# Optimization experiments

Measured on AMD Instinct MI355X. Metric: run time of the kernel, lower is better.

## Reference

```python
import jax, jax.numpy as jnp
import numpy as np

T_SEQ = 120
BATCH = 256
HID = 512
D_LAG = 32
D_COV = 32
D_OUT = 1
N_LAYERS = 2
D_IN0 = D_LAG + D_COV
BN_EPS = 1e-5
SCALE_EPS = 1e-6
GAMMA = 1.0


def _gru_layer(x, Wih, Whh, bih, bhh):
    # x: [B, T, D] -> [B, T, H]; PyTorch GRU gate order (r, z, n)
    H = Whh.shape[1]
    gx = jnp.einsum('btd,gd->btg', x, Wih) + bih  # [B, T, 3H]
    gx_t = jnp.swapaxes(gx, 0, 1)                 # [T, B, 3H]
    h0 = jnp.zeros((x.shape[0], H), x.dtype)

    def step(h, g):
        gh = h @ Whh.T + bhh
        r = jax.nn.sigmoid(g[:, :H] + gh[:, :H])
        z = jax.nn.sigmoid(g[:, H:2 * H] + gh[:, H:2 * H])
        n = jnp.tanh(g[:, 2 * H:] + r * gh[:, 2 * H:])
        h = (1.0 - z) * n + z * h
        return h, h

    _, hs = jax.lax.scan(step, h0, gx_t)
    return jnp.swapaxes(hs, 0, 1)  # [B, T, H]


def setup_inputs() -> dict:
    key = jax.random.key(0)
    ks = jax.random.split(key, 16)
    s = 1.0 / np.sqrt(HID)
    inp = {
        'X_emb': jnp.zeros((T_SEQ, BATCH, 1), dtype=jnp.int32),
        'X_cov': jax.random.normal(ks[0], (T_SEQ, BATCH, D_COV), dtype=jnp.float32),
        'X_lag': jax.random.normal(ks[1], (T_SEQ, BATCH, D_LAG), dtype=jnp.float32),
        'y': jax.random.normal(ks[2], (T_SEQ, BATCH, D_OUT), dtype=jnp.float32),
        'd_outputseqlen': 24,
        'len_win': 30,
        'W_ih0': jax.random.uniform(ks[3], (3 * HID, D_IN0), minval=-s, maxval=s),
        'W_hh0': jax.random.uniform(ks[4], (3 * HID, HID), minval=-s, maxval=s),
        'b_ih0': jax.random.uniform(ks[5], (3 * HID,), minval=-s, maxval=s),
        'b_hh0': jax.random.uniform(ks[6], (3 * HID,), minval=-s, maxval=s),
        'W_ih1': jax.random.uniform(ks[7], (3 * HID, HID), minval=-s, maxval=s),
        'W_hh1': jax.random.uniform(ks[8], (3 * HID, HID), minval=-s, maxval=s),
        'b_ih1': jax.random.uniform(ks[9], (3 * HID,), minval=-s, maxval=s),
        'b_hh1': jax.random.uniform(ks[10], (3 * HID,), minval=-s, maxval=s),
        'gate_W': jax.random.normal(ks[11], (N_LAYERS, T_SEQ, T_SEQ * 2 * HID)) * 0.05,
        'gate_b': jnp.zeros((N_LAYERS, T_SEQ)),
        'bn_gamma': jnp.ones((N_LAYERS, T_SEQ)),
        'bn_beta': jnp.zeros((N_LAYERS, T_SEQ)),
        'fc_W': jax.random.uniform(ks[12], (D_OUT, HID), minval=-s, maxval=s),
        'fc_b': jnp.zeros((D_OUT,)),
    }
    return inp


def reference(X_emb, X_cov, X_lag, y, d_outputseqlen, len_win,
              W_ih0, W_hh0, b_ih0, b_hh0, W_ih1, W_hh1, b_ih1, b_hh1,
              gate_W, gate_b, bn_gamma, bn_beta, fc_W, fc_b):
    T, B, _ = X_lag.shape
    half = B // 2
    x = jnp.concatenate([X_lag, X_cov], axis=-1)   # [T, B, D]
    x = jnp.transpose(x, (1, 0, 2))                # [B, T, D]

    gru_params = [(W_ih0, W_hh0, b_ih0, b_hh0), (W_ih1, W_hh1, b_ih1, b_hh1)]
    outs = []
    gate_weights = []
    for l, (Wih, Whh, bih, bhh) in enumerate(gru_params):
        x = _gru_layer(x, Wih, Whh, bih, bhh)      # [B, T, H]
        outs.append(x)
        # process_gate_weight: src/tgt halves concatenated on feature dim
        x_all = jnp.concatenate([x[:half], x[half:]], axis=2).reshape(half, -1)  # [B/2, T*2H]
        z = x_all @ gate_W[l].T + gate_b[l]        # [B/2, T]
        m = z.mean(axis=0)
        v = ((z - m) ** 2).mean(axis=0)            # biased var (BatchNorm training mode)
        w = jax.nn.sigmoid(bn_gamma[l] * (z - m) / jnp.sqrt(v + BN_EPS) + bn_beta[l])
        gate_weights.append(jax.nn.softmax(w.mean(axis=0)))  # [T]

    # prediction head (original uses fc_scale for both loc and scale)
    fea = outs[-1]
    lin = fea[:, -d_outputseqlen:, :] @ fc_W.T + fc_b          # [B, L, D_OUT]
    y_hat_loc = jnp.transpose(lin, (1, 0, 2))                  # [L, B, D_OUT]
    y_hat_scale = jnp.transpose(jax.nn.softplus(lin), (1, 0, 2)) + SCALE_EPS
    y_t = y[-d_outputseqlen:]
    log_prob = (-0.5 * ((y_t - y_hat_loc) / y_hat_scale) ** 2
                - jnp.log(y_hat_scale) - 0.5 * jnp.log(2.0 * jnp.pi))
    loss_y = -log_prob.mean()

    # linear-MMD transfer loss over windowed (j, k) pairs, all layers
    idx = jnp.arange(T)
    mask = (jnp.abs(idx[:, None] - idx[None, :]) <= len_win).astype(fea.dtype)  # [T, T]
    loss_transfer = jnp.zeros(())
    for l, o in enumerate(outs):
        ms = o[:half].mean(axis=0)   # [T, H]
        mt = o[half:].mean(axis=0)   # [T, H]
        # D[j,k] = ||ms[j]-mt[k]||^2 == linear MMD of columns j (src) and k (tgt)
        D = ((ms ** 2).sum(-1)[:, None] + (mt ** 2).sum(-1)[None, :]
             - 2.0 * ms @ mt.T)
        loss_transfer = loss_transfer + jnp.dot(gate_weights[l], (mask * D).sum(axis=1))
    total_loss = loss_y + GAMMA * loss_transfer
    return (total_loss, loss_y, y_hat_loc, y_hat_scale, jnp.stack(gate_weights))
```

## Files before the change

### kernel.cpp

```cpp
#include <hip/hip_runtime.h>
#include <math.h>

#define T_SEQ 120
#define BATCH 256
#define HID   512
#define G3    1536
#define MROWS (BATCH*T_SEQ)
#define TS    (T_SEQ*HID)
#define KGATE 122880
#define FSTRIDE 16
#define NEGINF (-2147483647)

typedef __attribute__((ext_vector_type(8))) short bf16x8;
typedef __attribute__((ext_vector_type(4))) float f32x4;

__device__ __forceinline__ unsigned short f2bf(float f) {
    union { float f; unsigned u; } x; x.f = f;
    unsigned r = x.u + 0x7fffu + ((x.u >> 16) & 1u);
    return (unsigned short)(r >> 16);
}
__device__ __forceinline__ float bf2f(unsigned short u) {
    union { unsigned u; float f; } x; x.u = ((unsigned)u) << 16; return x.f;
}
__device__ __forceinline__ float sigm_fast(float x) {
    return 1.f / (1.f + __expf(-x));
}
__device__ __forceinline__ float tanh_fast(float x) {
    float e = __expf(2.f * x);
    return 1.f - 2.f / (e + 1.f);
}

__global__ void build_x(const float* __restrict__ X_lag,
                        const float* __restrict__ X_cov,
                        float* __restrict__ x_in)
{
    int idx = blockIdx.x * 256 + threadIdx.x;
    int d = idx & 63;
    int m = idx >> 6;
    int b = m / 120, t = m - b * 120;
    float v;
    if (d < 32) v = X_lag[((size_t)t * BATCH + b) * 32 + d];
    else        v = X_cov[((size_t)t * BATCH + b) * 32 + (d - 32)];
    x_in[idx] = v;
}

__global__ void cast_whh0(const float* __restrict__ W, unsigned short* __restrict__ o)
{
    int i = blockIdx.x * 256 + threadIdx.x;
    o[i] = f2bf(W[i]);
}

__global__ void cast_wcat1(const float* __restrict__ Whh, const float* __restrict__ Wih,
                           unsigned short* __restrict__ o)
{
    int i = blockIdx.x * 256 + threadIdx.x;
    int row = i >> 10, c = i & 1023;
    float v = (c < 512) ? Whh[row * 512 + c] : Wih[row * 512 + (c - 512)];
    o[i] = f2bf(v);
}

__global__ void mkbias(const float* __restrict__ bih0, const float* __restrict__ bhh0,
                       const float* __restrict__ bih1, const float* __restrict__ bhh1,
                       float* __restrict__ bcomb0, float* __restrict__ bc1)
{
    int n = blockIdx.x * 256 + threadIdx.x;
    bcomb0[n] = bih0[n] + (n < 1024 ? bhh0[n] : 0.f);
    bc1[n]    = bih1[n] + (n < 1024 ? bhh1[n] : 0.f);
}

__global__ __launch_bounds__(256) void gemm_abt_t(
    const float* __restrict__ A, const float* __restrict__ B,
    const float* __restrict__ bias, unsigned short* __restrict__ C,
    int M, int N, int K)
{
    __shared__ float As[32][129];
    __shared__ float Bs[32][129];
    int m0 = blockIdx.x * 128;
    int n0 = blockIdx.y * 128;
    int tid = threadIdx.x;
    int tx = tid & 15, ty = tid >> 4;
    float acc[8][8] = {};
    for (int k0 = 0; k0 < K; k0 += 32) {
        #pragma unroll
        for (int i = 0; i < 16; i++) {
            int e = tid + i * 256;
            int row = e >> 5, col = e & 31;
            As[col][row] = A[(size_t)(m0 + row) * K + k0 + col];
            Bs[col][row] = B[(size_t)(n0 + row) * K + k0 + col];
        }
        __syncthreads();
        #pragma unroll
        for (int kk = 0; kk < 32; kk++) {
            float a[8], b[8];
            #pragma unroll
            for (int i = 0; i < 8; i++) a[i] = As[kk][ty + i * 16];
            #pragma unroll
            for (int j = 0; j < 8; j++) b[j] = Bs[kk][tx + j * 16];
            #pragma unroll
            for (int i = 0; i < 8; i++)
                #pragma unroll
                for (int j = 0; j < 8; j++) acc[i][j] += a[i] * b[j];
        }
        __syncthreads();
    }
    #pragma unroll
    for (int i = 0; i < 8; i++) {
        int m = m0 + ty + i * 16;
        int b = m / 120, t = m - b * 120;
        #pragma unroll
        for (int j = 0; j < 8; j++) {
            int n = n0 + tx + j * 16;
            C[((size_t)t * 256 + b) * G3 + n] = f2bf(acc[i][j] + bias[n]);
        }
    }
}

__device__ __forceinline__ bool wait2(const int* __restrict__ f0b,
                                      const int* __restrict__ f1b,
                                      int thr0, int thr1, int lane)
{
    const int* ap; int thr;
    if (lane < 16)      { ap = f0b + lane * FSTRIDE;        thr = thr0; }
    else if (lane < 32) { ap = f1b + (lane - 16) * FSTRIDE; thr = thr1; }
    else                { ap = f0b;                         thr = NEGINF; }
    for (int it = 0; it < 50000; ++it) {
        int v = __hip_atomic_load(ap, __ATOMIC_RELAXED, __HIP_MEMORY_SCOPE_AGENT);
        if (__all(v >= thr)) return true;
        __builtin_amdgcn_s_sleep(1);
    }
    return false;
}

__global__ __launch_bounds__(256) void gru_xcd(
    const unsigned short* __restrict__ gx0,
    const unsigned short* __restrict__ Whh0,
    const unsigned short* __restrict__ Wcat1,
    const float* __restrict__ bhh0,
    const float* __restrict__ bc1,
    const float* __restrict__ bhh1,
    unsigned short* __restrict__ out0,
    unsigned short* __restrict__ out1,
    int* __restrict__ flags,
    int* __restrict__ rolecnt)
{
    __shared__ unsigned short wlds[96 * 520];
    __shared__ int role_s;

    int xcd;
    asm("s_getreg_b32 %0, hwreg(20, 0, 32)" : "=s"(xcd));
    xcd &= 7;
    if (threadIdx.x == 0) role_s = atomicAdd(&rolecnt[xcd * 16], 1);
    __syncthreads();
    const int role = role_s;
    if (role >= 32) return;

    const int layer = role >> 4;
    const int jb    = role & 15;
    const int j0    = jb * 32;
    const int tid   = threadIdx.x;
    const int w     = tid >> 6, lane = tid & 63;
    const int l15   = lane & 15, l4 = lane >> 4;
    const int jt    = w & 1, bt = w >> 1;
    const int jloc  = jt * 16 + l15;
    const int j     = j0 + jloc;
    const int bloc0 = bt * 16;
    const int bg0   = xcd * 32;

    {
        const unsigned short* Wsrc = layer ? Wcat1 : Whh0;
        const int wstr = layer ? 1024 : 512;
        for (int c = tid; c < 96 * 64; c += 256) {
            int lr = c >> 6, ck = c & 63;
            int grow = (lr >> 5) * 512 + j0 + (lr & 31);
            bf16x8 v = *(const bf16x8*)(Wsrc + (size_t)grow * wstr + ck * 8);
            *(bf16x8*)&wlds[lr * 520 + ck * 8] = v;
        }
    }
    float bn_, br_ = 0.f, bz_ = 0.f, bnx_ = 0.f;
    if (layer) { br_ = bc1[j]; bz_ = bc1[512 + j]; bnx_ = bc1[1024 + j]; bn_ = bhh1[1024 + j]; }
    else       { bn_ = bhh0[1024 + j]; }
    float carry[4] = {0.f, 0.f, 0.f, 0.f};

    const int* f0b = flags + (0 * 8 + xcd) * 16 * FSTRIDE;
    const int* f1b = flags + (1 * 8 + xcd) * 16 * FSTRIDE;
    int* myf = flags + ((layer * 8 + xcd) * 16 + jb) * FSTRIDE;
    __syncthreads();

    for (int t = 0; t < T_SEQ; t++) {
        bool ok = layer ? wait2(f0b, f1b, t, t - 1, lane)
                        : wait2(f0b, f1b, t - 1, NEGINF, lane);
        if (!ok) break;

        f32x4 a0 = {0,0,0,0}, a1 = {0,0,0,0}, a2 = {0,0,0,0}, a3 = {0,0,0,0};
        if (t > 0) {
            const unsigned short* hp = layer ? out1 : out0;
            #pragma unroll
            for (int ks = 0; ks < 16; ks++) {
                const int ko = ks * 32 + 8 * l4;
                bf16x8 A = *(const bf16x8*)(hp + ((size_t)(bg0 + bloc0 + l15) * T_SEQ + (t - 1)) * 512 + ko);
                bf16x8 B0 = *(const bf16x8*)&wlds[(0 * 32 + jloc) * 520 + ko];
                bf16x8 B1 = *(const bf16x8*)&wlds[(1 * 32 + jloc) * 520 + ko];
                bf16x8 B2 = *(const bf16x8*)&wlds[(2 * 32 + jloc) * 520 + ko];
                a0 = __builtin_amdgcn_mfma_f32_16x16x32_bf16(A, B0, a0, 0, 0, 0);
                a1 = __builtin_amdgcn_mfma_f32_16x16x32_bf16(A, B1, a1, 0, 0, 0);
                a2 = __builtin_amdgcn_mfma_f32_16x16x32_bf16(A, B2, a2, 0, 0, 0);
            }
        }
        if (layer) {
            #pragma unroll
            for (int ks = 0; ks < 16; ks++) {
                const int ko = ks * 32 + 8 * l4;
                bf16x8 A = *(const bf16x8*)(out0 + ((size_t)(bg0 + bloc0 + l15) * T_SEQ + t) * 512 + ko);
                const unsigned short* wb = Wcat1 + (size_t)j * 1024 + 512 + ko;
                bf16x8 B0 = *(const bf16x8*)(wb);
                bf16x8 B1 = *(const bf16x8*)(wb + 512 * 1024);
                bf16x8 B2 = *(const bf16x8*)(wb + 1024 * 1024);
                a0 = __builtin_amdgcn_mfma_f32_16x16x32_bf16(A, B0, a0, 0, 0, 0);
                a1 = __builtin_amdgcn_mfma_f32_16x16x32_bf16(A, B1, a1, 0, 0, 0);
                a3 = __builtin_amdgcn_mfma_f32_16x16x32_bf16(A, B2, a3, 0, 0, 0);
            }
        }
        unsigned short* op = layer ? out1 : out0;
        #pragma unroll
        for (int rr = 0; rr < 4; rr++) {
            int b = bg0 + bloc0 + 4 * l4 + rr;
            float pr, pz, pnx;
            if (!layer) {
                const unsigned short* gp = gx0 + ((size_t)t * 256 + b) * G3 + j;
                pr  = bf2f(gp[0])    + a0[rr];
                pz  = bf2f(gp[512])  + a1[rr];
                pnx = bf2f(gp[1024]);
            } else {
                pr = a0[rr] + br_; pz = a1[rr] + bz_; pnx = a3[rr] + bnx_;
            }
            float r = sigm_fast(pr);
            float z = sigm_fast(pz);
            float n = tanh_fast(pnx + r * (a2[rr] + bn_));
            float h = (1.f - z) * n + z * carry[rr];
            carry[rr] = h;
            op[((size_t)b * T_SEQ + t) * 512 + j] = f2bf(h);
        }
        asm volatile("s_waitcnt vmcnt(0)" ::: "memory");
        __syncthreads();
        if (tid == 0)
            __hip_atomic_store(myf, t, __ATOMIC_RELAXED, __HIP_MEMORY_SCOPE_AGENT);
    }
}

__global__ __launch_bounds__(256) void zpart_kernel(
    const unsigned short* __restrict__ out, const float* __restrict__ Gw,
    float* __restrict__ zp)
{
    __shared__ float Os[128][33];
    __shared__ float Gs[128][33];
    int bk = blockIdx.x;
    int t = bk >> 3, half = (bk >> 2) & 1, cq = bk & 3;
    int tid = threadIdx.x;
    int tx = tid & 15, ty = tid >> 4;
    float acc[8][8] = {};
    int cbase = cq * 128;
    for (int c0 = cbase; c0 < cbase + 128; c0 += 32) {
        #pragma unroll
        for (int i = 0; i < 16; i++) {
            int e = tid + i * 256;
            int row = e >> 5, col = e & 31;
            Os[row][col] = bf2f(out[((size_t)(row + half * 128) * T_SEQ + t) * 512 + c0 + col]);
            float v = 0.f;
            if (row < 120)
                v = Gw[(size_t)row * KGATE + (size_t)t * 1024 + half * 512 + c0 + col];
            Gs[row][col] = v;
        }
        __syncthreads();
        #pragma unroll
        for (int kk = 0; kk < 32; kk++) {
            float a[8], g[8];
            #pragma unroll
            for (int i = 0; i < 8; i++) a[i] = Os[ty + i * 16][kk];
            #pragma unroll
            for (int j = 0; j < 8; j++) g[j] = Gs[tx + j * 16][kk];
            #pragma unroll
            for (int i = 0; i < 8; i++)
                #pragma unroll
                for (int j = 0; j < 8; j++) acc[i][j] += a[i] * g[j];
        }
        __syncthreads();
    }
    float* zb = zp + (size_t)bk * (128 * 120);
    #pragma unroll
    for (int i = 0; i < 8; i++) {
        int ii = ty + i * 16;
        #pragma unroll
        for (int j = 0; j < 8; j++) {
            int r = tx + j * 16;
            if (r < 120) zb[ii * 120 + r] = acc[i][j];
        }
    }
}

__global__ void zreduce(const float* __restrict__ zp,
                        const float* __restrict__ gate_b_l,
                        float* __restrict__ z)
{
    int idx = blockIdx.x * 256 + threadIdx.x;
    if (idx >= 128 * 120) return;
    float s = 0.f;
    for (int c = 0; c < 960; c++) s += zp[(size_t)c * (128 * 120) + idx];
    z[idx] = s + gate_b_l[idx % 120];
}

__global__ __launch_bounds__(128) void bn_col(
    const float* __restrict__ z, const float* __restrict__ gamma,
    const float* __restrict__ beta, float* __restrict__ wm)
{
    int r = blockIdx.x, i = threadIdx.x;
    __shared__ float sh[2];
    float v = z[i * 120 + r];
    float s = v;
    for (int o = 32; o > 0; o >>= 1) s += __shfl_down(s, o);
    if ((i & 63) == 0) sh[i >> 6] = s;
    __syncthreads();
    float m = (sh[0] + sh[1]) * (1.f / 128.f);
    __syncthreads();
    float d = (v - m) * (v - m);
    for (int o = 32; o > 0; o >>= 1) d += __shfl_down(d, o);
    if ((i & 63) == 0) sh[i >> 6] = d;
    __syncthreads();
    float var = (sh[0] + sh[1]) * (1.f / 128.f);
    float w = 1.f / (1.f + expf(-(gamma[r] * (v - m) / sqrtf(var + 1e-5f) + beta[r])));
    __syncthreads();
    float ws_ = w;
    for (int o = 32; o > 0; o >>= 1) ws_ += __shfl_down(ws_, o);
    if ((i & 63) == 0) sh[i >> 6] = ws_;
    __syncthreads();
    if (i == 0) wm[r] = (sh[0] + sh[1]) * (1.f / 128.f);
}

__global__ __launch_bounds__(128) void softmax120(
    const float* __restrict__ wm, float* __restrict__ g_out,
    float* __restrict__ g_ws)
{
    int i = threadIdx.x;
    __shared__ float sh[2];
    float v = (i < 120) ? wm[i] : -1e30f;
    float m = v;
    for (int o = 32; o > 0; o >>= 1) m = fmaxf(m, __shfl_down(m, o));
    if ((i & 63) == 0) sh[i >> 6] = m;
    __syncthreads();
    float mx = fmaxf(sh[0], sh[1]);
    float e = (i < 120) ? expf(v - mx) : 0.f;
    __syncthreads();
    float se = e;
    for (int o = 32; o > 0; o >>= 1) se += __shfl_down(se, o);
    if ((i & 63) == 0) sh[i >> 6] = se;
    __syncthreads();
    float sum = sh[0] + sh[1];
    if (i < 120) { float g = e / sum; g_out[i] = g; g_ws[i] = g; }
}

__global__ void halfmeans(const unsigned short* __restrict__ out,
                          float* __restrict__ ms, float* __restrict__ mt)
{
    int idx = blockIdx.x * 256 + threadIdx.x;
    int half = idx >= TS;
    int tc = idx - half * TS;
    const unsigned short* base = out + (size_t)(half * 128) * TS + tc;
    float s = 0.f;
    for (int i = 0; i < 128; i++) s += bf2f(base[(size_t)i * TS]);
    s *= (1.f / 128.f);
    if (half) mt[tc] = s; else ms[tc] = s;
}

__global__ __launch_bounds__(512) void transfer_part(
    const float* __restrict__ ms, const float* __restrict__ mt,
    const float* __restrict__ gw, const int* __restrict__ lenw,
    float* __restrict__ part)
{
    int t = blockIdx.x, c = threadIdx.x;
    int lw = lenw[0];
    int j0 = t - lw; if (j0 < 0) j0 = 0;
    int j1 = t + lw; if (j1 > 119) j1 = 119;
    float m_c = ms[(size_t)t * 512 + c];
    float acc = 0.f;
    for (int j = j0; j <= j1; j++) {
        float d = m_c - mt[(size_t)j * 512 + c];
        acc += d * d;
    }
    for (int o = 32; o > 0; o >>= 1) acc += __shfl_down(acc, o);
    __shared__ float sh[8];
    if ((c & 63) == 0) sh[c >> 6] = acc;
    __syncthreads();
    if (c == 0) {
        float s = 0.f;
        #pragma unroll
        for (int k = 0; k < 8; k++) s += sh[k];
        part[t] = gw[t] * s;
    }
}

__global__ __launch_bounds__(256) void yhat_kernel(
    const unsigned short* __restrict__ out1, const float* __restrict__ y,
    const float* __restrict__ fcW, const float* __restrict__ fcb,
    int dsl, float* __restrict__ dout, float* __restrict__ lp_rows)
{
    int wid = blockIdx.x * 4 + (threadIdx.x >> 6);
    int lane = threadIdx.x & 63;
    int tt = wid >> 8, b = wid & 255;
    int t = T_SEQ - dsl + tt;
    const unsigned short* row = out1 + ((size_t)b * T_SEQ + t) * 512;
    float s = 0.f;
    #pragma unroll
    for (int k = 0; k < 8; k++) s += bf2f(row[lane + 64 * k]) * fcW[lane + 64 * k];
    for (int o = 32; o > 0; o >>= 1) s += __shfl_down(s, o);
    if (lane == 0) {
        float loc = s + fcb[0];
        float sp = fmaxf(loc, 0.f) + log1pf(expf(-fabsf(loc)));
        float scale = sp + 1e-6f;
        dout[2 + tt * 256 + b] = loc;
        dout[2 + dsl * 256 + tt * 256 + b] = scale;
        float yt = y[(size_t)t * 256 + b];
        float u = (yt - loc) / scale;
        lp_rows[wid] = -0.5f * u * u - logf(scale) - 0.91893853320467274f;
    }
}

__global__ __launch_bounds__(64) void finalize(
    const float* __restrict__ lp_rows, const float* __restrict__ part0,
    const float* __restrict__ part1, float* __restrict__ dout, int n_lp)
{
    int i = threadIdx.x;
    float s = 0.f;
    for (int k = i; k < n_lp; k += 64) s += lp_rows[k];
    for (int o = 32; o > 0; o >>= 1) s += __shfl_down(s, o);
    float tr = 0.f;
    for (int k = i; k < 120; k += 64) tr += part0[k] + part1[k];
    for (int o = 32; o > 0; o >>= 1) tr += __shfl_down(tr, o);
    if (i == 0) {
        float ly = -s / (float)n_lp;
        dout[1] = ly;
        dout[0] = ly + tr;
    }
}

extern "C" void kernel_launch(void* const* d_in, const int* in_sizes, int n_in,
                              void* d_out, int out_size, void* d_ws, size_t ws_size,
                              hipStream_t stream)
{
    const float* X_cov  = (const float*)d_in[1];
    const float* X_lag  = (const float*)d_in[2];
    const float* y      = (const float*)d_in[3];
    const int*   lenw   = (const int*)d_in[5];
    const float* W_ih0  = (const float*)d_in[6];
    const float* W_hh0  = (const float*)d_in[7];
    const float* b_ih0  = (const float*)d_in[8];
    const float* b_hh0  = (const float*)d_in[9];
    const float* W_ih1  = (const float*)d_in[10];
    const float* W_hh1  = (const float*)d_in[11];
    const float* b_ih1  = (const float*)d_in[12];
    const float* b_hh1  = (const float*)d_in[13];
    const float* gate_W = (const float*)d_in[14];
    const float* gate_b = (const float*)d_in[15];
    const float* bn_g   = (const float*)d_in[16];
    const float* bn_b   = (const float*)d_in[17];
    const float* fc_W   = (const float*)d_in[18];
    const float* fc_b   = (const float*)d_in[19];
    float* dout = (float*)d_out;
    float* ws   = (float*)d_ws;

    float* x_in    = ws;
    unsigned short* gx0bf = (unsigned short*)(ws + 1966080);
    unsigned short* out0  = (unsigned short*)(ws + 25559040);
    unsigned short* out1  = (unsigned short*)(ws + 33423360);
    unsigned short* Whh0bf  = (unsigned short*)(ws + 41287680);
    unsigned short* Wcat1bf = (unsigned short*)(ws + 41680896);
    float* zmat    = ws + 42467328;
    float* wm      = ws + 42482688;
    float* gw_ws   = ws + 42482808;
    float* msb     = ws + 42483048;
    float* mtb     = ws + 42544488;
    float* part    = ws + 42605928;
    float* bcomb0  = ws + 42606168;
    float* bc1     = ws + 42607704;
    int*   flags   = (int*)(ws + 42609240);
    int*   rolecnt = (int*)(ws + 42613336);
    float* zp      = ws + 1966080;
    float* lp_rows = x_in;

    int dsl = (out_size - 2 - 2 * T_SEQ) / (2 * BATCH);

    build_x<<<dim3(7680), 256, 0, stream>>>(X_lag, X_cov, x_in);
    cast_whh0<<<dim3(3072), 256, 0, stream>>>(W_hh0, Whh0bf);
    cast_wcat1<<<dim3(6144), 256, 0, stream>>>(W_hh1, W_ih1, Wcat1bf);
    mkbias<<<dim3(6), 256, 0, stream>>>(b_ih0, b_hh0, b_ih1, b_hh1, bcomb0, bc1);
    hipMemsetAsync(flags, 0xFF, 4096 * sizeof(int), stream);
    hipMemsetAsync(rolecnt, 0, 128 * sizeof(int), stream);

    gemm_abt_t<<<dim3(240, 12), 256, 0, stream>>>(x_in, W_ih0, bcomb0, gx0bf,
                                                  MROWS, G3, 64);

    gru_xcd<<<dim3(320), 256, 0, stream>>>(gx0bf, Whh0bf, Wcat1bf,
                                           b_hh0, bc1, b_hh1,
                                           out0, out1, flags, rolecnt);

    for (int l = 0; l < 2; l++) {
        const unsigned short* o = l ? out1 : out0;
        zpart_kernel<<<960, 256, 0, stream>>>(o, gate_W + (size_t)l * 120 * KGATE, zp);
        zreduce<<<60, 256, 0, stream>>>(zp, gate_b + l * 120, zmat);
        bn_col<<<120, 128, 0, stream>>>(zmat, bn_g + l * 120, bn_b + l * 120, wm);
        softmax120<<<1, 128, 0, stream>>>(wm, dout + 2 + 2 * dsl * 256 + l * 120,
                                          gw_ws + l * 120);
        halfmeans<<<480, 256, 0, stream>>>(o, msb, mtb);
        transfer_part<<<120, 512, 0, stream>>>(msb, mtb, gw_ws + l * 120, lenw,
                                               part + l * 120);
    }

    yhat_kernel<<<dsl * 64, 256, 0, stream>>>(out1, y, fc_W, fc_b, dsl, dout, lp_rows);
    finalize<<<1, 64, 0, stream>>>(lp_rows, part, part + 120, dout, dsl * 256);
}
```

Before: 1.898 ms.

## Split GRU layer loops and overlap recurrent matmul with cross-layer waits

The persistent GRU kernel gets separate loops per layer. Layer 0 now prefetches its gx gate values before spinning on the flag. Layer 1 waits only on its own layer's previous step, runs the recurrent h@Whh MFMAs, and only then waits on layer 0's current step before the input-projection MFMAs. The A operands are loaded into a register array before the MFMA chain. The aim is to hide the cross-layer dependency latency and global-load latency behind useful work, at the cost of higher register pressure and more code.

```diff
diff --git a/kernel.cpp b/kernel.cpp
--- a/kernel.cpp
+++ b/kernel.cpp
@@ -9,7 +9,6 @@
 #define TS    (T_SEQ*HID)
 #define KGATE 122880
 #define FSTRIDE 16
-#define NEGINF (-2147483647)
 
 typedef __attribute__((ext_vector_type(8))) short bf16x8;
 typedef __attribute__((ext_vector_type(4))) float f32x4;
@@ -115,15 +114,10 @@
     }
 }
 
-__device__ __forceinline__ bool wait2(const int* __restrict__ f0b,
-                                      const int* __restrict__ f1b,
-                                      int thr0, int thr1, int lane)
-{
-    const int* ap; int thr;
-    if (lane < 16)      { ap = f0b + lane * FSTRIDE;        thr = thr0; }
-    else if (lane < 32) { ap = f1b + (lane - 16) * FSTRIDE; thr = thr1; }
-    else                { ap = f0b;                         thr = NEGINF; }
-    for (int it = 0; it < 50000; ++it) {
+__device__ __forceinline__ bool wait16(const int* __restrict__ fb, int thr, int lane)
+{
+    const int* ap = fb + (lane & 15) * FSTRIDE;
+    for (int it = 0; it < 100000; ++it) {
         int v = __hip_atomic_load(ap, __ATOMIC_RELAXED, __HIP_MEMORY_SCOPE_AGENT);
         if (__all(v >= thr)) return true;
         __builtin_amdgcn_s_sleep(1);
@@ -186,64 +180,104 @@
     int* myf = flags + ((layer * 8 + xcd) * 16 + jb) * FSTRIDE;
     __syncthreads();
 
-    for (int t = 0; t < T_SEQ; t++) {
-        bool ok = layer ? wait2(f0b, f1b, t, t - 1, lane)
-                        : wait2(f0b, f1b, t - 1, NEGINF, lane);
-        if (!ok) break;
-
-        f32x4 a0 = {0,0,0,0}, a1 = {0,0,0,0}, a2 = {0,0,0,0}, a3 = {0,0,0,0};
-        if (t > 0) {
-            const unsigned short* hp = layer ? out1 : out0;
-            #pragma unroll
-            for (int ks = 0; ks < 16; ks++) {
-                const int ko = ks * 32 + 8 * l4;
-                bf16x8 A = *(const bf16x8*)(hp + ((size_t)(bg0 + bloc0 + l15) * T_SEQ + (t - 1)) * 512 + ko);
-                bf16x8 B0 = *(const bf16x8*)&wlds[(0 * 32 + jloc) * 520 + ko];
-                bf16x8 B1 = *(const bf16x8*)&wlds[(1 * 32 + jloc) * 520 + ko];
-                bf16x8 B2 = *(const bf16x8*)&wlds[(2 * 32 + jloc) * 520 + ko];
-                a0 = __builtin_amdgcn_mfma_f32_16x16x32_bf16(A, B0, a0, 0, 0, 0);
-                a1 = __builtin_amdgcn_mfma_f32_16x16x32_bf16(A, B1, a1, 0, 0, 0);
-                a2 = __builtin_amdgcn_mfma_f32_16x16x32_bf16(A, B2, a2, 0, 0, 0);
+    if (!layer) {
+        for (int t = 0; t < T_SEQ; t++) {
+            unsigned short gr_[4], gz_[4], gn_[4];
+            #pragma unroll
+            for (int rr = 0; rr < 4; rr++) {
+                int b = bg0 + bloc0 + 4 * l4 + rr;
+                const unsigned short* gp = gx0 + ((size_t)t * 256 + b) * G3 + j;
+                gr_[rr] = gp[0]; gz_[rr] = gp[512]; gn_[rr] = gp[1024];
             }
-        }
-        if (layer) {
-            #pragma unroll
-            for (int ks = 0; ks < 16; ks++) {
-                const int ko = ks * 32 + 8 * l4;
-                bf16x8 A = *(const bf16x8*)(out0 + ((size_t)(bg0 + bloc0 + l15) * T_SEQ + t) * 512 + ko);
-                const unsigned short* wb = Wcat1 + (size_t)j * 1024 + 512 + ko;
-                bf16x8 B0 = *(const bf16x8*)(wb);
-                bf16x8 B1 = *(const bf16x8*)(wb + 512 * 1024);
-                bf16x8 B2 = *(const bf16x8*)(wb + 1024 * 1024);
-                a0 = __builtin_amdgcn_mfma_f32_16x16x32_bf16(A, B0, a0, 0, 0, 0);
-                a1 = __builtin_amdgcn_mfma_f32_16x16x32_bf16(A, B1, a1, 0, 0, 0);
-                a3 = __builtin_amdgcn_mfma_f32_16x16x32_bf16(A, B2, a3, 0, 0, 0);
+            asm volatile("" ::: "memory");
+
+            if (!wait16(f0b, t - 1, lane)) break;
+
+            f32x4 a0 = {0,0,0,0}, a1 = {0,0,0,0}, a2 = {0,0,0,0};
+            if (t > 0) {
+                bf16x8 Areg[16];
+                #pragma unroll
+                for (int ks = 0; ks < 16; ks++)
+                    Areg[ks] = *(const bf16x8*)(out0 + ((size_t)(bg0 + bloc0 + l15) * T_SEQ + (t - 1)) * 512 + ks * 32 + 8 * l4);
+                #pragma unroll
+                for (int ks = 0; ks < 16; ks++) {
+                    const int ko = ks * 32 + 8 * l4;
+                    bf16x8 B0 = *(const bf16x8*)&wlds[(0 * 32 + jloc) * 520 + ko];
+                    bf16x8 B1 = *(const bf16x8*)&wlds[(1 * 32 + jloc) * 520 + ko];
+                    bf16x8 B2 = *(const bf16x8*)&wlds[(2 * 32 + jloc) * 520 + ko];
+                    a0 = __builtin_amdgcn_mfma_f32_16x16x32_bf16(Areg[ks], B0, a0, 0, 0, 0);
+                    a1 = __builtin_amdgcn_mfma_f32_16x16x32_bf16(Areg[ks], B1, a1, 0, 0, 0);
+                    a2 = __builtin_amdgcn_mfma_f32_16x16x32_bf16(Areg[ks], B2, a2, 0, 0, 0);
+                }
             }
-        }
-        unsigned short* op = layer ? out1 : out0;
-        #pragma unroll
-        for (int rr = 0; rr < 4; rr++) {
-            int b = bg0 + bloc0 + 4 * l4 + rr;
-            float pr, pz, pnx;
-            if (!layer) {
-                const unsigned short* gp = gx0 + ((size_t)t * 256 + b) * G3 + j;
-                pr  = bf2f(gp[0])    + a0[rr];
-                pz  = bf2f(gp[512])  + a1[rr];
-                pnx = bf2f(gp[1024]);
-            } else {
-                pr = a0[rr] + br_; pz = a1[rr] + bz_; pnx = a3[rr] + bnx_;
+            #pragma unroll
+            for (int rr = 0; rr < 4; rr++) {
+                int b = bg0 + bloc0 + 4 * l4 + rr;
+                float r = sigm_fast(bf2f(gr_[rr]) + a0[rr]);
+                float z = sigm_fast(bf2f(gz_[rr]) + a1[rr]);
+                float n = tanh_fast(bf2f(gn_[rr]) + r * (a2[rr] + bn_));
+                float h = (1.f - z) * n + z * carry[rr];
+                carry[rr] = h;
+                out0[((size_t)b * T_SEQ + t) * 512 + j] = f2bf(h);
             }
-            float r = sigm_fast(pr);
-            float z = sigm_fast(pz);
-            float n = tanh_fast(pnx + r * (a2[rr] + bn_));
-            float h = (1.f - z) * n + z * carry[rr];
-            carry[rr] = h;
-            op[((size_t)b * T_SEQ + t) * 512 + j] = f2bf(h);
-        }
-        asm volatile("s_waitcnt vmcnt(0)" ::: "memory");
-        __syncthreads();
-        if (tid == 0)
-            __hip_atomic_store(myf, t, __ATOMIC_RELAXED, __HIP_MEMORY_SCOPE_AGENT);
+            asm volatile("s_waitcnt vmcnt(0)" ::: "memory");
+            __syncthreads();
+            if (tid == 0)
+                __hip_atomic_store(myf, t, __ATOMIC_RELAXED, __HIP_MEMORY_SCOPE_AGENT);
+        }
+    } else {
+        for (int t = 0; t < T_SEQ; t++) {
+            f32x4 a0 = {0,0,0,0}, a1 = {0,0,0,0}, a2 = {0,0,0,0}, a3 = {0,0,0,0};
+            if (!wait16(f1b, t - 1, lane)) break;
+            if (t > 0) {
+                bf16x8 Areg[16];
+                #pragma unroll
+                for (int ks = 0; ks < 16; ks++)
+                    Areg[ks] = *(const bf16x8*)(out1 + ((size_t)(bg0 + bloc0 + l15) * T_SEQ + (t - 1)) * 512 + ks * 32 + 8 * l4);
+                #pragma unroll
+                for (int ks = 0; ks < 16; ks++) {
+                    const int ko = ks * 32 + 8 * l4;
+                    bf16x8 B0 = *(const bf16x8*)&wlds[(0 * 32 + jloc) * 520 + ko];
+                    bf16x8 B1 = *(const bf16x8*)&wlds[(1 * 32 + jloc) * 520 + ko];
+                    bf16x8 B2 = *(const bf16x8*)&wlds[(2 * 32 + jloc) * 520 + ko];
+                    a0 = __builtin_amdgcn_mfma_f32_16x16x32_bf16(Areg[ks], B0, a0, 0, 0, 0);
+                    a1 = __builtin_amdgcn_mfma_f32_16x16x32_bf16(Areg[ks], B1, a1, 0, 0, 0);
+                    a2 = __builtin_amdgcn_mfma_f32_16x16x32_bf16(Areg[ks], B2, a2, 0, 0, 0);
+                }
+            }
+            if (!wait16(f0b, t, lane)) break;
+            {
+                bf16x8 Areg[16];
+                #pragma unroll
+                for (int ks = 0; ks < 16; ks++)
+                    Areg[ks] = *(const bf16x8*)(out0 + ((size_t)(bg0 + bloc0 + l15) * T_SEQ + t) * 512 + ks * 32 + 8 * l4);
+                #pragma unroll
+                for (int ks = 0; ks < 16; ks++) {
+                    const int ko = ks * 32 + 8 * l4;
+                    const unsigned short* wb = Wcat1 + (size_t)j * 1024 + 512 + ko;
+                    bf16x8 B0 = *(const bf16x8*)(wb);
+                    bf16x8 B1 = *(const bf16x8*)(wb + 512 * 1024);
+                    bf16x8 B2 = *(const bf16x8*)(wb + 1024 * 1024);
+                    a0 = __builtin_amdgcn_mfma_f32_16x16x32_bf16(Areg[ks], B0, a0, 0, 0, 0);
+                    a1 = __builtin_amdgcn_mfma_f32_16x16x32_bf16(Areg[ks], B1, a1, 0, 0, 0);
+                    a3 = __builtin_amdgcn_mfma_f32_16x16x32_bf16(Areg[ks], B2, a3, 0, 0, 0);
+                }
+            }
+            #pragma unroll
+            for (int rr = 0; rr < 4; rr++) {
+                int b = bg0 + bloc0 + 4 * l4 + rr;
+                float r = sigm_fast(a0[rr] + br_);
+                float z = sigm_fast(a1[rr] + bz_);
+                float n = tanh_fast(a3[rr] + bnx_ + r * (a2[rr] + bn_));
+                float h = (1.f - z) * n + z * carry[rr];
+                carry[rr] = h;
+                out1[((size_t)b * T_SEQ + t) * 512 + j] = f2bf(h);
+            }
+            asm volatile("s_waitcnt vmcnt(0)" ::: "memory");
+            __syncthreads();
+            if (tid == 0)
+                __hip_atomic_store(myf, t, __ATOMIC_RELAXED, __HIP_MEMORY_SCOPE_AGENT);
+        }
     }
 }
 
```

New measurement: 1.893 ms. About the same (-0.2%).
